# Kernel tuning notes

Hardware: AMD Instinct MI355X
Metric: run time of the kernel (lower is better)

The kernel has to match this reference:

```python
import jax, jax.numpy as jnp
import numpy as np

N = 50000
E = 1600000
IN_C = 165
HID = 256
HEADS = 8
OUT_C = 2
NEG_SLOPE = 0.2


def setup_inputs() -> dict:
    key = jax.random.key(0)
    ks = jax.random.split(key, 10)
    x = jax.random.normal(ks[0], (N, IN_C), dtype=jnp.float32)
    edge_index = jax.random.randint(ks[1], (2, E), 0, N, dtype=jnp.int64)
    c1 = HID // HEADS  # 32 per-head channels in layer 1
    W1 = jax.random.normal(ks[2], (IN_C, HEADS * c1), dtype=jnp.float32) * (1.0 / np.sqrt(IN_C))
    att_src1 = jax.random.normal(ks[3], (HEADS, c1), dtype=jnp.float32) * 0.1
    att_dst1 = jax.random.normal(ks[4], (HEADS, c1), dtype=jnp.float32) * 0.1
    b1 = jnp.zeros((HEADS * c1,), dtype=jnp.float32)
    W2 = jax.random.normal(ks[5], (HID, 1 * OUT_C), dtype=jnp.float32) * (1.0 / np.sqrt(HID))
    att_src2 = jax.random.normal(ks[6], (1, OUT_C), dtype=jnp.float32) * 0.1
    att_dst2 = jax.random.normal(ks[7], (1, OUT_C), dtype=jnp.float32) * 0.1
    b2 = jnp.zeros((OUT_C,), dtype=jnp.float32)
    return {"x": x, "edge_index": edge_index, "W1": W1, "att_src1": att_src1,
            "att_dst1": att_dst1, "b1": b1, "W2": W2, "att_src2": att_src2,
            "att_dst2": att_dst2, "b2": b2}


def _gat_conv(x, src, dst, W, att_src, att_dst, bias, heads, concat):
    """PyG GATConv (eval mode, self-loops already appended to src/dst)."""
    n = x.shape[0]
    c = att_src.shape[1]
    h = (x @ W).reshape(n, heads, c)                      # [N, H, C]
    a_src = jnp.einsum('nhc,hc->nh', h, att_src)          # [N, H]
    a_dst = jnp.einsum('nhc,hc->nh', h, att_dst)
    e = a_src[src] + a_dst[dst]                           # [Et, H]
    e = jax.nn.leaky_relu(e, NEG_SLOPE)
    # segment softmax over incoming edges of each dst node
    e_max = jax.ops.segment_max(e, dst, num_segments=n)   # [N, H]
    e_exp = jnp.exp(e - e_max[dst])
    denom = jax.ops.segment_sum(e_exp, dst, num_segments=n)
    alpha = e_exp / denom[dst]                            # [Et, H]
    msg = alpha[:, :, None] * h[src]                      # [Et, H, C]
    out = jax.ops.segment_sum(msg, dst, num_segments=n)   # [N, H, C]
    if concat:
        out = out.reshape(n, heads * c)
    else:
        out = out.mean(axis=1)
    return out + bias


def reference(x, edge_index, W1, att_src1, att_dst1, b1, W2, att_src2, att_dst2, b2):
    n = x.shape[0]
    loops = jnp.arange(n, dtype=edge_index.dtype)
    src = jnp.concatenate([edge_index[0], loops])  # add_self_loops=True (PyG default)
    dst = jnp.concatenate([edge_index[1], loops])
    h = _gat_conv(x, src, dst, W1, att_src1, att_dst1, b1, HEADS, True)
    h = jax.nn.elu(h)
    out = _gat_conv(h, src, dst, W2, att_src2, att_dst2, b2, 1, False)
    return out
```

## Files before the change

### kernel.cpp

```cpp
#include <hip/hip_runtime.h>
#include <hip/hip_bf16.h>
#include <math.h>

#define N_NODES 50000
#define N_EDGES 1600000
#define ET (N_EDGES + N_NODES)
#define IN_C 165
#define HID 256
#define HEADS 8
#define C1 32
#define OUT_C 2
#define NEG_SLOPE 0.2f
#define LOG2E 1.44269504088896f
#define TROWS 32
#define XSTR 36
#define GEMM_BLOCKS ((N_NODES + TROWS - 1) / TROWS)
#define SCB 2048
#define SGRP 256
#define NPP ((N_NODES + 7) / 8)
#define CAPL 96
#define NE4 (N_EDGES / 4)
#define CK 8
#define NCH 21

typedef float f32x2 __attribute__((ext_vector_type(2)));

__device__ inline float lrelu(float v) { return v > 0.f ? v : NEG_SLOPE * v; }
__device__ inline float e2l(float t) { return exp2f(fmaxf(t, NEG_SLOPE * t)); }

__device__ inline unsigned short f32_bf16(float f) {
    unsigned u = __float_as_uint(f);
    return (unsigned short)((u + 0x7FFFu + ((u >> 16) & 1u)) >> 16);
}

__device__ inline float bflo(unsigned u) { return __uint_as_float(u << 16); }
__device__ inline float bfhi(unsigned u) { return __uint_as_float(u & 0xFFFF0000u); }

__device__ __forceinline__ void gemm1_att_block(
        int row0, const float* __restrict__ x, const float* __restrict__ W,
        const float* __restrict__ att_src, const float* __restrict__ att_dst,
        unsigned short* __restrict__ h, float* __restrict__ a_src,
        float* __restrict__ a_dst, float* xs, float* wb) {
    const int tid = threadIdx.x;
    const int nrow = (N_NODES - row0 < TROWS) ? (N_NODES - row0) : TROWS;
    const int lim = nrow * IN_C;
    for (int idx = tid; idx < TROWS * IN_C; idx += 256) {
        int r = idx / IN_C, k = idx - r * IN_C;
        xs[k * XSTR + r] = (idx < lim) ? x[(size_t)row0 * IN_C + idx] : 0.f;
    }
    const int u  = tid & 31;
    const int kr = tid >> 5;
    {
        const float* wsrc = W + (size_t)kr * HID + u * 8;
        float4 pa = *(const float4*)(wsrc);
        float4 pb = *(const float4*)(wsrc + 4);
        *(float4*)(wb + (kr * 64 + u) * 4)      = pa;
        *(float4*)(wb + (kr * 64 + u + 32) * 4) = pb;
    }
    __syncthreads();

    const int tr = tid >> 5;
    const int cq = tid & 31;
    const int c0 = cq * 8;
    float acc[4][8];
    #pragma unroll
    for (int j = 0; j < 4; ++j)
        #pragma unroll
        for (int q = 0; q < 8; ++q) acc[j][q] = 0.f;

    #pragma unroll 2
    for (int c = 0; c < NCH - 1; ++c) {
        int krow = (c + 1) * CK + kr;
        if (krow > IN_C - 1) krow = IN_C - 1;
        const float* wsrc = W + (size_t)krow * HID + u * 8;
        float4 pa = *(const float4*)(wsrc);
        float4 pb = *(const float4*)(wsrc + 4);
        const float* wcur = wb + (c & 1) * (CK * 256);
        const int k0 = c * CK;
        #pragma unroll
        for (int kk = 0; kk < CK; ++kk) {
            float4 xc = *(const float4*)(xs + (k0 + kk) * XSTR + tr * 4);
            float4 a0 = *(const float4*)(wcur + (kk * 64 + cq) * 4);
            float4 a1 = *(const float4*)(wcur + (kk * 64 + cq + 32) * 4);
            #pragma unroll
            for (int j = 0; j < 4; ++j) {
                float xj = (j == 0) ? xc.x : (j == 1) ? xc.y : (j == 2) ? xc.z : xc.w;
                acc[j][0] += xj * a0.x; acc[j][1] += xj * a0.y;
                acc[j][2] += xj * a0.z; acc[j][3] += xj * a0.w;
                acc[j][4] += xj * a1.x; acc[j][5] += xj * a1.y;
                acc[j][6] += xj * a1.z; acc[j][7] += xj * a1.w;
            }
        }
        float* wn = wb + ((c + 1) & 1) * (CK * 256);
        *(float4*)(wn + (kr * 64 + u) * 4)      = pa;
        *(float4*)(wn + (kr * 64 + u + 32) * 4) = pb;
        __syncthreads();
    }
    {
        const float* wcur = wb + ((NCH - 1) & 1) * (CK * 256);
        const int k0 = (NCH - 1) * CK;
        #pragma unroll
        for (int kk = 0; kk < IN_C - (NCH - 1) * CK; ++kk) {
            float4 xc = *(const float4*)(xs + (k0 + kk) * XSTR + tr * 4);
            float4 a0 = *(const float4*)(wcur + (kk * 64 + cq) * 4);
            float4 a1 = *(const float4*)(wcur + (kk * 64 + cq + 32) * 4);
            #pragma unroll
            for (int j = 0; j < 4; ++j) {
                float xj = (j == 0) ? xc.x : (j == 1) ? xc.y : (j == 2) ? xc.z : xc.w;
                acc[j][0] += xj * a0.x; acc[j][1] += xj * a0.y;
                acc[j][2] += xj * a0.z; acc[j][3] += xj * a0.w;
                acc[j][4] += xj * a1.x; acc[j][5] += xj * a1.y;
                acc[j][6] += xj * a1.z; acc[j][7] += xj * a1.w;
            }
        }
    }
    #pragma unroll
    for (int j = 0; j < 4; ++j) {
        int gr = row0 + tr * 4 + j;
        if (gr < N_NODES) {
            unsigned p[4];
            #pragma unroll
            for (int q = 0; q < 4; ++q)
                p[q] = (unsigned)f32_bf16(acc[j][2*q]) |
                       ((unsigned)f32_bf16(acc[j][2*q+1]) << 16);
            *(uint4*)(h + (size_t)gr * HID + c0) = make_uint4(p[0], p[1], p[2], p[3]);
        }
    }
    {
        const int hd = cq >> 2;
        const float* as = att_src + hd * C1 + (cq & 3) * 8;
        const float* ad = att_dst + hd * C1 + (cq & 3) * 8;
        float av[8], dv[8];
        #pragma unroll
        for (int q = 0; q < 2; ++q) {
            float4 a4 = *(const float4*)(as + q * 4);
            float4 d4 = *(const float4*)(ad + q * 4);
            av[q*4+0]=a4.x; av[q*4+1]=a4.y; av[q*4+2]=a4.z; av[q*4+3]=a4.w;
            dv[q*4+0]=d4.x; dv[q*4+1]=d4.y; dv[q*4+2]=d4.z; dv[q*4+3]=d4.w;
        }
        float ps[4], pd[4];
        #pragma unroll
        for (int j = 0; j < 4; ++j) {
            float s = 0.f, d = 0.f;
            #pragma unroll
            for (int q = 0; q < 8; ++q) {
                s += acc[j][q] * av[q];
                d += acc[j][q] * dv[q];
            }
            ps[j] = s; pd[j] = d;
        }
        #pragma unroll
        for (int off = 1; off <= 2; off <<= 1) {
            #pragma unroll
            for (int j = 0; j < 4; ++j) {
                ps[j] += __shfl_xor(ps[j], off);
                pd[j] += __shfl_xor(pd[j], off);
            }
        }
        if ((cq & 3) == 0) {
            #pragma unroll
            for (int j = 0; j < 4; ++j) {
                int gr = row0 + tr * 4 + j;
                if (gr < N_NODES) {
                    a_src[gr * 8 + hd] = ps[j] * LOG2E;
                    a_dst[gr * 8 + hd] = pd[j] * LOG2E;
                }
            }
        }
    }
}

__global__ __launch_bounds__(256) void fusedAB_kernel(
        const float* __restrict__ x, const float* __restrict__ W,
        const float* __restrict__ att_src, const float* __restrict__ att_dst,
        unsigned short* __restrict__ h, float* __restrict__ a_src,
        float* __restrict__ a_dst,
        const int* __restrict__ src, const int* __restrict__ dst,
        int* __restrict__ deg, unsigned short* __restrict__ csr) {
    __shared__ float xs[IN_C * XSTR];
    __shared__ float wlds[2 * CK * 256];
    if (blockIdx.x < GEMM_BLOCKS) {
        gemm1_att_block(blockIdx.x * TROWS, x, W, att_src, att_dst,
                        h, a_src, a_dst, xs, wlds);
    } else {
        const int sb  = blockIdx.x - GEMM_BLOCKS;
        const int cls = sb & 7;
        const int blk = sb >> 3;
        const int lo = cls * NPP;
        const int hi = (lo + NPP < N_NODES) ? lo + NPP : N_NODES;
        const int t = blk * 256 + threadIdx.x;
        if (t < hi - lo) {
            int d = lo + t;
            int slot = atomicAdd(&deg[d], 1);
            csr[(size_t)d * CAPL + slot] = (unsigned short)d;
        }
        const int4* dst4 = (const int4*)dst;
        for (int uu = t; uu < NE4; uu += SGRP * 256) {
            int4 dv = dst4[uu];
            #pragma unroll
            for (int j = 0; j < 4; ++j) {
                int d = (j == 0) ? dv.x : (j == 1) ? dv.y : (j == 2) ? dv.z : dv.w;
                if (d >= lo && d < hi) {
                    int slot = atomicAdd(&deg[d], 1);
                    csr[(size_t)d * CAPL + slot] = (unsigned short)src[4 * uu + j];
                }
            }
        }
    }
}

__global__ __launch_bounds__(256) void agg1_fused_kernel(
        const int* __restrict__ deg, const unsigned short* __restrict__ csr,
        const float* __restrict__ a_src, const float* __restrict__ a_dst,
        const unsigned short* __restrict__ h1, const float* __restrict__ bias1,
        const float* __restrict__ W2,
        const float* __restrict__ as2, const float* __restrict__ ad2,
        float4* __restrict__ pk, float* __restrict__ a2d) {
    int wid = (blockIdx.x * 256 + threadIdx.x) >> 6;
    int l = threadIdx.x & 63;
    if (wid >= N_NODES) return;
    const int el = l >> 5;
    const int q  = l & 31;
    const int hd = q >> 2;
    const int ch = q * 8;
    const unsigned short* lst = csr + (size_t)wid * CAPL;
    const int n = deg[wid];
    const float ad_p = a_dst[wid * 8 + hd];
    float den = 0.f;
    f32x2 ac0 = {0.f, 0.f}, ac1 = {0.f, 0.f}, ac2 = {0.f, 0.f}, ac3 = {0.f, 0.f};
    int i = 0;
    for (; i + 16 <= n; i += 16) {
        int s[8];
        #pragma unroll
        for (int j = 0; j < 8; ++j) s[j] = lst[i + 2 * j + el];
        uint4 v[8];
        #pragma unroll
        for (int j = 0; j < 8; ++j)
            v[j] = *(const uint4*)(h1 + (size_t)s[j] * HID + ch);
        float w[8];
        #pragma unroll
        for (int j = 0; j < 8; ++j)
            w[j] = e2l(a_src[s[j] * 8 + hd] + ad_p);
        #pragma unroll
        for (int j = 0; j < 8; ++j) {
            den += w[j];
            f32x2 w2 = {w[j], w[j]};
            ac0 += w2 * (f32x2){bflo(v[j].x), bfhi(v[j].x)};
            ac1 += w2 * (f32x2){bflo(v[j].y), bfhi(v[j].y)};
            ac2 += w2 * (f32x2){bflo(v[j].z), bfhi(v[j].z)};
            ac3 += w2 * (f32x2){bflo(v[j].w), bfhi(v[j].w)};
        }
    }
    for (; i < n; i += 8) {
        int s[4]; float mk[4];
        #pragma unroll
        for (int j = 0; j < 4; ++j) {
            int e = i + 2 * j + el;
            mk[j] = (e < n) ? 1.f : 0.f;
            s[j] = lst[(e < n) ? e : (n - 1)];
        }
        uint4 v[4];
        #pragma unroll
        for (int j = 0; j < 4; ++j)
            v[j] = *(const uint4*)(h1 + (size_t)s[j] * HID + ch);
        float w[4];
        #pragma unroll
        for (int j = 0; j < 4; ++j)
            w[j] = mk[j] * e2l(a_src[s[j] * 8 + hd] + ad_p);
        #pragma unroll
        for (int j = 0; j < 4; ++j) {
            den += w[j];
            f32x2 w2 = {w[j], w[j]};
            ac0 += w2 * (f32x2){bflo(v[j].x), bfhi(v[j].x)};
            ac1 += w2 * (f32x2){bflo(v[j].y), bfhi(v[j].y)};
            ac2 += w2 * (f32x2){bflo(v[j].z), bfhi(v[j].z)};
            ac3 += w2 * (f32x2){bflo(v[j].w), bfhi(v[j].w)};
        }
    }
    float accs[8] = {ac0.x, ac0.y, ac1.x, ac1.y, ac2.x, ac2.y, ac3.x, ac3.y};
    den += __shfl_xor(den, 32);
    #pragma unroll
    for (int k = 0; k < 8; ++k) accs[k] += __shfl_xor(accs[k], 32);

    const float inv = 1.f / den;
    float4 bva = *(const float4*)(bias1 + ch);
    float4 bvb = *(const float4*)(bias1 + ch + 4);
    float o[8];
    o[0] = accs[0] * inv + bva.x; o[1] = accs[1] * inv + bva.y;
    o[2] = accs[2] * inv + bva.z; o[3] = accs[3] * inv + bva.w;
    o[4] = accs[4] * inv + bvb.x; o[5] = accs[5] * inv + bvb.y;
    o[6] = accs[6] * inv + bvb.z; o[7] = accs[7] * inv + bvb.w;
    #pragma unroll
    for (int k = 0; k < 8; ++k) o[k] = o[k] > 0.f ? o[k] : expm1f(o[k]);
    const float* wv = W2 + q * 16;
    float4 w0 = *(const float4*)(wv);
    float4 w1 = *(const float4*)(wv + 4);
    float4 w2 = *(const float4*)(wv + 8);
    float4 w3 = *(const float4*)(wv + 12);
    float p0 = o[0]*w0.x + o[1]*w0.z + o[2]*w1.x + o[3]*w1.z
             + o[4]*w2.x + o[5]*w2.z + o[6]*w3.x + o[7]*w3.z;
    float p1 = o[0]*w0.y + o[1]*w0.w + o[2]*w1.y + o[3]*w1.w
             + o[4]*w2.y + o[5]*w2.w + o[6]*w3.y + o[7]*w3.w;
    #pragma unroll
    for (int off = 16; off; off >>= 1) {
        p0 += __shfl_xor(p0, off);
        p1 += __shfl_xor(p1, off);
    }
    if (l == 0) {
        pk[wid] = make_float4(p0, p1, (p0 * as2[0] + p1 * as2[1]) * LOG2E, 0.f);
        a2d[wid] = (p0 * ad2[0] + p1 * ad2[1]) * LOG2E;
    }
}

__global__ __launch_bounds__(256) void agg2_fused_kernel(
        const int* __restrict__ deg, const unsigned short* __restrict__ csr,
        const float4* __restrict__ pk, const float* __restrict__ a2d,
        const float* __restrict__ b2, float* __restrict__ out) {
    int t = blockIdx.x * 256 + threadIdx.x;
    int node = t >> 4;
    int l = t & 15;
    if (node >= N_NODES) return;
    const unsigned short* lst = csr + (size_t)node * CAPL;
    const int n = deg[node];
    const float adv = a2d[node];
    float sm = 0.f, acc0 = 0.f, acc1 = 0.f;
    for (int i = l; i < n; i += 64) {
        int s[4]; float mk[4];
        #pragma unroll
        for (int j = 0; j < 4; ++j) {
            int e = i + 16 * j;
            mk[j] = (e < n) ? 1.f : 0.f;
            s[j] = lst[(e < n) ? e : (n - 1)];
        }
        float4 pv[4];
        #pragma unroll
        for (int j = 0; j < 4; ++j) pv[j] = pk[s[j]];
        #pragma unroll
        for (int j = 0; j < 4; ++j) {
            float w = mk[j] * e2l(pv[j].z + adv);
            sm += w;
            acc0 += w * pv[j].x;
            acc1 += w * pv[j].y;
        }
    }
    #pragma unroll
    for (int off = 8; off; off >>= 1) {
        sm   += __shfl_xor(sm, off);
        acc0 += __shfl_xor(acc0, off);
        acc1 += __shfl_xor(acc1, off);
    }
    if (l == 0) {
        *(float2*)(out + node * 2) =
            make_float2(acc0 / sm + b2[0], acc1 / sm + b2[1]);
    }
}

extern "C" void kernel_launch(void* const* d_in, const int* in_sizes, int n_in,
                              void* d_out, int out_size, void* d_ws, size_t ws_size,
                              hipStream_t stream) {
    (void)in_sizes; (void)n_in; (void)out_size; (void)ws_size;
    const float* x        = (const float*)d_in[0];
    const int*   ei       = (const int*)d_in[1];
    const float* W1       = (const float*)d_in[2];
    const float* att_src1 = (const float*)d_in[3];
    const float* att_dst1 = (const float*)d_in[4];
    const float* b1       = (const float*)d_in[5];
    const float* W2       = (const float*)d_in[6];
    const float* att_src2 = (const float*)d_in[7];
    const float* att_dst2 = (const float*)d_in[8];
    const float* b2       = (const float*)d_in[9];
    float* out = (float*)d_out;

    const int* src = ei;
    const int* dst = ei + N_EDGES;

    char* ws = (char*)d_ws;
    size_t off = 0;
    unsigned short* h1 = (unsigned short*)(ws + off);
    off += (size_t)N_NODES * HID * 2;
    float* a_src1 = (float*)(ws + off); off += (size_t)N_NODES * HEADS * 4;
    float* a_dst1 = (float*)(ws + off); off += (size_t)N_NODES * HEADS * 4;
    float4* pk = (float4*)(ws + off); off += (size_t)N_NODES * 16;
    float* a2d = (float*)(ws + off); off += (size_t)N_NODES * 4;
    int* deg    = (int*)(ws + off); off += (size_t)N_NODES * 4;
    unsigned short* csr = (unsigned short*)(ws + off);
    off += (size_t)N_NODES * CAPL * 2;

    hipMemsetAsync(deg, 0, (size_t)N_NODES * 4, stream);

    const int NW = (N_NODES * 64 + 255) / 256;

    fusedAB_kernel<<<GEMM_BLOCKS + SCB, 256, 0, stream>>>(
        x, W1, att_src1, att_dst1, h1, a_src1, a_dst1, src, dst, deg, csr);

    agg1_fused_kernel<<<NW, 256, 0, stream>>>(
        deg, csr, a_src1, a_dst1, h1, b1, W2, att_src2, att_dst2, pk, a2d);

    agg2_fused_kernel<<<(N_NODES * 16 + 255) / 256, 256, 0, stream>>>(
        deg, csr, pk, a2d, b2, out);
}
```

Before: 338.9 us.

## Replace FP32 scalar layer-1 GEMM with split-bf16 MFMA and folded attention projections

Moves the x@W1 GEMM from FP32 FMA loops to 32x32x16 bf16 MFMA instructions. Both operands are split into hi and lo bf16 parts and three products are summed to stay close to FP32 accuracy. A new prep kernel packs W1 into an MFMA fragment layout. It also precomputes W1·att_src and W1·att_dst so the attention logits come from an extra MFMA on one wave, not from a reduction over the output. This costs an extra kernel launch, a per-block x split in LDS, and uncoalesced scalar bf16 stores of h.

```diff
diff --git a/kernel.cpp b/kernel.cpp
--- a/kernel.cpp
+++ b/kernel.cpp
@@ -13,17 +13,24 @@
 #define NEG_SLOPE 0.2f
 #define LOG2E 1.44269504088896f
 #define TROWS 32
-#define XSTR 36
 #define GEMM_BLOCKS ((N_NODES + TROWS - 1) / TROWS)
 #define SCB 2048
 #define SGRP 256
 #define NPP ((N_NODES + 7) / 8)
 #define CAPL 96
 #define NE4 (N_EDGES / 4)
-#define CK 8
-#define NCH 21
+
+#define NSTEP 11
+#define BIMG_BYTES ((size_t)NSTEP * 16384)
+#define WAIMG_BYTES ((size_t)NSTEP * 2048)
+#define WT (NSTEP * 512)
+#define WPB ((WT + 255) / 256)
+#define WAT (176 * 16)
+#define WAB ((WAT + 255) / 256)
 
 typedef float f32x2 __attribute__((ext_vector_type(2)));
+typedef short s16x8 __attribute__((ext_vector_type(8)));
+typedef float f32x16 __attribute__((ext_vector_type(16)));
 
 __device__ inline float lrelu(float v) { return v > 0.f ? v : NEG_SLOPE * v; }
 __device__ inline float e2l(float t) { return exp2f(fmaxf(t, NEG_SLOPE * t)); }
@@ -35,153 +42,165 @@
 
 __device__ inline float bflo(unsigned u) { return __uint_as_float(u << 16); }
 __device__ inline float bfhi(unsigned u) { return __uint_as_float(u & 0xFFFF0000u); }
-
-__device__ __forceinline__ void gemm1_att_block(
-        int row0, const float* __restrict__ x, const float* __restrict__ W,
+__device__ inline float bf2f(unsigned short b) { return __uint_as_float(((unsigned)b) << 16); }
+
+__global__ __launch_bounds__(256) void prep_kernel(
+        const float* __restrict__ W,
         const float* __restrict__ att_src, const float* __restrict__ att_dst,
+        unsigned short* __restrict__ bImg, unsigned short* __restrict__ waImg) {
+    if (blockIdx.x < WPB) {
+        int g2 = blockIdx.x * 256 + threadIdx.x;
+        if (g2 >= WT) return;
+        int s = g2 >> 9;
+        int r9 = g2 & 511;
+        int kg = r9 >> 8, nsub = (r9 >> 5) & 7, c32 = r9 & 31;
+        int col = nsub * 32 + c32;
+        int k0 = s * 16 + kg * 8;
+        unsigned short hb[8], lb[8];
+        #pragma unroll
+        for (int i = 0; i < 8; ++i) {
+            int k = k0 + i;
+            float v = (k < IN_C) ? W[(size_t)k * HID + col] : 0.f;
+            hb[i] = f32_bf16(v);
+            lb[i] = f32_bf16(v - bf2f(hb[i]));
+        }
+        unsigned ph[4], pl[4];
+        #pragma unroll
+        for (int q = 0; q < 4; ++q) {
+            ph[q] = (unsigned)hb[2*q] | ((unsigned)hb[2*q+1] << 16);
+            pl[q] = (unsigned)lb[2*q] | ((unsigned)lb[2*q+1] << 16);
+        }
+        unsigned short* base = bImg + (size_t)s * 8192
+                             + ((nsub * 2 + kg) * 32 + c32) * 8;
+        *(uint4*)(base)        = make_uint4(ph[0], ph[1], ph[2], ph[3]);
+        *(uint4*)(base + 4096) = make_uint4(pl[0], pl[1], pl[2], pl[3]);
+    } else {
+        int g2 = (blockIdx.x - WPB) * 256 + threadIdx.x;
+        if (g2 >= WAT) return;
+        int k = g2 >> 4, j = g2 & 15;
+        int head = j >> 1;
+        float dotv = 0.f;
+        if (k < IN_C) {
+            const float* wr = W + (size_t)k * HID + head * 32;
+            const float* at = ((j & 1) ? att_dst : att_src) + head * 32;
+            #pragma unroll
+            for (int c = 0; c < 32; c += 4) {
+                float4 wv = *(const float4*)(wr + c);
+                float4 av = *(const float4*)(at + c);
+                dotv += wv.x*av.x + wv.y*av.y + wv.z*av.z + wv.w*av.w;
+            }
+        }
+        unsigned short dh = f32_bf16(dotv);
+        unsigned short dl = f32_bf16(dotv - bf2f(dh));
+        int s = k >> 4, kk = k & 15, kg = kk >> 3, i = kk & 7;
+        unsigned short* base = waImg + (size_t)s * 1024 + (kg * 32 + j) * 8 + i;
+        base[0]   = dh;
+        base[512] = dl;
+    }
+}
+
+__device__ __forceinline__ void gemm_mfma_block(
+        int b, const float* __restrict__ x,
+        const unsigned short* __restrict__ bImg,
+        const unsigned short* __restrict__ waImg,
         unsigned short* __restrict__ h, float* __restrict__ a_src,
-        float* __restrict__ a_dst, float* xs, float* wb) {
+        float* __restrict__ a_dst, unsigned short* asr) {
     const int tid = threadIdx.x;
-    const int nrow = (N_NODES - row0 < TROWS) ? (N_NODES - row0) : TROWS;
-    const int lim = nrow * IN_C;
-    for (int idx = tid; idx < TROWS * IN_C; idx += 256) {
-        int r = idx / IN_C, k = idx - r * IN_C;
-        xs[k * XSTR + r] = (idx < lim) ? x[(size_t)row0 * IN_C + idx] : 0.f;
-    }
-    const int u  = tid & 31;
-    const int kr = tid >> 5;
-    {
-        const float* wsrc = W + (size_t)kr * HID + u * 8;
-        float4 pa = *(const float4*)(wsrc);
-        float4 pb = *(const float4*)(wsrc + 4);
-        *(float4*)(wb + (kr * 64 + u) * 4)      = pa;
-        *(float4*)(wb + (kr * 64 + u + 32) * 4) = pb;
+    const int w = tid >> 6, l = tid & 63;
+    const int half = l >> 5, ln = l & 31;
+    const int row0 = b * TROWS;
+    for (int g = tid; g < 704; g += 256) {
+        int o = g >> 5, row = g & 31;
+        int s = o >> 1, kg = o & 1;
+        int node = row0 + row;
+        int k0 = o * 8;
+        unsigned short hb[8], lb[8];
+        #pragma unroll
+        for (int i = 0; i < 8; ++i) {
+            int k = k0 + i;
+            float v = (node < N_NODES && k < IN_C) ? x[(size_t)node * IN_C + k] : 0.f;
+            hb[i] = f32_bf16(v);
+            lb[i] = f32_bf16(v - bf2f(hb[i]));
+        }
+        unsigned ph[4], pl[4];
+        #pragma unroll
+        for (int q = 0; q < 4; ++q) {
+            ph[q] = (unsigned)hb[2*q] | ((unsigned)hb[2*q+1] << 16);
+            pl[q] = (unsigned)lb[2*q] | ((unsigned)lb[2*q+1] << 16);
+        }
+        unsigned short* base = asr + s * 1024 + (kg * 32 + row) * 8;
+        *(uint4*)(base)       = make_uint4(ph[0], ph[1], ph[2], ph[3]);
+        *(uint4*)(base + 512) = make_uint4(pl[0], pl[1], pl[2], pl[3]);
     }
     __syncthreads();
 
-    const int tr = tid >> 5;
-    const int cq = tid & 31;
-    const int c0 = cq * 8;
-    float acc[4][8];
-    #pragma unroll
-    for (int j = 0; j < 4; ++j)
-        #pragma unroll
-        for (int q = 0; q < 8; ++q) acc[j][q] = 0.f;
-
-    #pragma unroll 2
-    for (int c = 0; c < NCH - 1; ++c) {
-        int krow = (c + 1) * CK + kr;
-        if (krow > IN_C - 1) krow = IN_C - 1;
-        const float* wsrc = W + (size_t)krow * HID + u * 8;
-        float4 pa = *(const float4*)(wsrc);
-        float4 pb = *(const float4*)(wsrc + 4);
-        const float* wcur = wb + (c & 1) * (CK * 256);
-        const int k0 = c * CK;
-        #pragma unroll
-        for (int kk = 0; kk < CK; ++kk) {
-            float4 xc = *(const float4*)(xs + (k0 + kk) * XSTR + tr * 4);
-            float4 a0 = *(const float4*)(wcur + (kk * 64 + cq) * 4);
-            float4 a1 = *(const float4*)(wcur + (kk * 64 + cq + 32) * 4);
-            #pragma unroll
-            for (int j = 0; j < 4; ++j) {
-                float xj = (j == 0) ? xc.x : (j == 1) ? xc.y : (j == 2) ? xc.z : xc.w;
-                acc[j][0] += xj * a0.x; acc[j][1] += xj * a0.y;
-                acc[j][2] += xj * a0.z; acc[j][3] += xj * a0.w;
-                acc[j][4] += xj * a1.x; acc[j][5] += xj * a1.y;
-                acc[j][6] += xj * a1.z; acc[j][7] += xj * a1.w;
+    f32x16 acc0, acc1, accA;
+    #pragma unroll
+    for (int r = 0; r < 16; ++r) { acc0[r] = 0.f; acc1[r] = 0.f; accA[r] = 0.f; }
+    const int ns0 = 2 * w, ns1 = 2 * w + 1;
+    const int afo = (half * 32 + ln) * 8;
+    const int fo0 = ((ns0 * 2 + half) * 32 + ln) * 8;
+    const int fo1 = ((ns1 * 2 + half) * 32 + ln) * 8;
+    for (int s = 0; s < NSTEP; ++s) {
+        const unsigned short* ab = asr + s * 1024;
+        s16x8 a_h = *(const s16x8*)(ab + afo);
+        s16x8 a_l = *(const s16x8*)(ab + 512 + afo);
+        const unsigned short* bb = bImg + (size_t)s * 8192;
+        s16x8 bh0 = *(const s16x8*)(bb + fo0);
+        s16x8 bh1 = *(const s16x8*)(bb + fo1);
+        s16x8 bl0 = *(const s16x8*)(bb + 4096 + fo0);
+        s16x8 bl1 = *(const s16x8*)(bb + 4096 + fo1);
+        acc0 = __builtin_amdgcn_mfma_f32_32x32x16_bf16(a_h, bh0, acc0, 0, 0, 0);
+        acc1 = __builtin_amdgcn_mfma_f32_32x32x16_bf16(a_h, bh1, acc1, 0, 0, 0);
+        acc0 = __builtin_amdgcn_mfma_f32_32x32x16_bf16(a_h, bl0, acc0, 0, 0, 0);
+        acc1 = __builtin_amdgcn_mfma_f32_32x32x16_bf16(a_h, bl1, acc1, 0, 0, 0);
+        acc0 = __builtin_amdgcn_mfma_f32_32x32x16_bf16(a_l, bh0, acc0, 0, 0, 0);
+        acc1 = __builtin_amdgcn_mfma_f32_32x32x16_bf16(a_l, bh1, acc1, 0, 0, 0);
+        if (w == 0) {
+            const unsigned short* wb = waImg + (size_t)s * 1024;
+            s16x8 wah = *(const s16x8*)(wb + afo);
+            s16x8 wal = *(const s16x8*)(wb + 512 + afo);
+            accA = __builtin_amdgcn_mfma_f32_32x32x16_bf16(a_h, wah, accA, 0, 0, 0);
+            accA = __builtin_amdgcn_mfma_f32_32x32x16_bf16(a_h, wal, accA, 0, 0, 0);
+            accA = __builtin_amdgcn_mfma_f32_32x32x16_bf16(a_l, wah, accA, 0, 0, 0);
+        }
+    }
+    #pragma unroll
+    for (int t = 0; t < 2; ++t) {
+        const int colg = w * 64 + t * 32 + ln;
+        #pragma unroll
+        for (int r = 0; r < 16; ++r) {
+            int row = (r & 3) + 8 * (r >> 2) + 4 * half;
+            int gr = row0 + row;
+            if (gr < N_NODES) {
+                float a = t ? acc1[r] : acc0[r];
+                h[(size_t)gr * HID + colg] = f32_bf16(a);
             }
         }
-        float* wn = wb + ((c + 1) & 1) * (CK * 256);
-        *(float4*)(wn + (kr * 64 + u) * 4)      = pa;
-        *(float4*)(wn + (kr * 64 + u + 32) * 4) = pb;
-        __syncthreads();
-    }
-    {
-        const float* wcur = wb + ((NCH - 1) & 1) * (CK * 256);
-        const int k0 = (NCH - 1) * CK;
-        #pragma unroll
-        for (int kk = 0; kk < IN_C - (NCH - 1) * CK; ++kk) {
-            float4 xc = *(const float4*)(xs + (k0 + kk) * XSTR + tr * 4);
-            float4 a0 = *(const float4*)(wcur + (kk * 64 + cq) * 4);
-            float4 a1 = *(const float4*)(wcur + (kk * 64 + cq + 32) * 4);
-            #pragma unroll
-            for (int j = 0; j < 4; ++j) {
-                float xj = (j == 0) ? xc.x : (j == 1) ? xc.y : (j == 2) ? xc.z : xc.w;
-                acc[j][0] += xj * a0.x; acc[j][1] += xj * a0.y;
-                acc[j][2] += xj * a0.z; acc[j][3] += xj * a0.w;
-                acc[j][4] += xj * a1.x; acc[j][5] += xj * a1.y;
-                acc[j][6] += xj * a1.z; acc[j][7] += xj * a1.w;
-            }
-        }
-    }
-    #pragma unroll
-    for (int j = 0; j < 4; ++j) {
-        int gr = row0 + tr * 4 + j;
-        if (gr < N_NODES) {
-            unsigned p[4];
-            #pragma unroll
-            for (int q = 0; q < 4; ++q)
-                p[q] = (unsigned)f32_bf16(acc[j][2*q]) |
-                       ((unsigned)f32_bf16(acc[j][2*q+1]) << 16);
-            *(uint4*)(h + (size_t)gr * HID + c0) = make_uint4(p[0], p[1], p[2], p[3]);
-        }
-    }
-    {
-        const int hd = cq >> 2;
-        const float* as = att_src + hd * C1 + (cq & 3) * 8;
-        const float* ad = att_dst + hd * C1 + (cq & 3) * 8;
-        float av[8], dv[8];
-        #pragma unroll
-        for (int q = 0; q < 2; ++q) {
-            float4 a4 = *(const float4*)(as + q * 4);
-            float4 d4 = *(const float4*)(ad + q * 4);
-            av[q*4+0]=a4.x; av[q*4+1]=a4.y; av[q*4+2]=a4.z; av[q*4+3]=a4.w;
-            dv[q*4+0]=d4.x; dv[q*4+1]=d4.y; dv[q*4+2]=d4.z; dv[q*4+3]=d4.w;
-        }
-        float ps[4], pd[4];
-        #pragma unroll
-        for (int j = 0; j < 4; ++j) {
-            float s = 0.f, d = 0.f;
-            #pragma unroll
-            for (int q = 0; q < 8; ++q) {
-                s += acc[j][q] * av[q];
-                d += acc[j][q] * dv[q];
-            }
-            ps[j] = s; pd[j] = d;
-        }
-        #pragma unroll
-        for (int off = 1; off <= 2; off <<= 1) {
-            #pragma unroll
-            for (int j = 0; j < 4; ++j) {
-                ps[j] += __shfl_xor(ps[j], off);
-                pd[j] += __shfl_xor(pd[j], off);
-            }
-        }
-        if ((cq & 3) == 0) {
-            #pragma unroll
-            for (int j = 0; j < 4; ++j) {
-                int gr = row0 + tr * 4 + j;
-                if (gr < N_NODES) {
-                    a_src[gr * 8 + hd] = ps[j] * LOG2E;
-                    a_dst[gr * 8 + hd] = pd[j] * LOG2E;
-                }
-            }
+    }
+    if (w == 0 && ln < 16) {
+        int head = ln >> 1;
+        float* ap = (ln & 1) ? a_dst : a_src;
+        #pragma unroll
+        for (int r = 0; r < 16; ++r) {
+            int row = (r & 3) + 8 * (r >> 2) + 4 * half;
+            int gr = row0 + row;
+            if (gr < N_NODES) ap[gr * 8 + head] = accA[r] * LOG2E;
         }
     }
 }
 
 __global__ __launch_bounds__(256) void fusedAB_kernel(
-        const float* __restrict__ x, const float* __restrict__ W,
-        const float* __restrict__ att_src, const float* __restrict__ att_dst,
+        const float* __restrict__ x,
+        const unsigned short* __restrict__ bImg,
+        const unsigned short* __restrict__ waImg,
         unsigned short* __restrict__ h, float* __restrict__ a_src,
         float* __restrict__ a_dst,
         const int* __restrict__ src, const int* __restrict__ dst,
         int* __restrict__ deg, unsigned short* __restrict__ csr) {
-    __shared__ float xs[IN_C * XSTR];
-    __shared__ float wlds[2 * CK * 256];
+    __shared__ unsigned short asr[NSTEP * 1024];
     if (blockIdx.x < GEMM_BLOCKS) {
-        gemm1_att_block(blockIdx.x * TROWS, x, W, att_src, att_dst,
-                        h, a_src, a_dst, xs, wlds);
+        gemm_mfma_block(blockIdx.x, x, bImg, waImg, h, a_src, a_dst, asr);
     } else {
         const int sb  = blockIdx.x - GEMM_BLOCKS;
         const int cls = sb & 7;
@@ -385,13 +404,17 @@
     int* deg    = (int*)(ws + off); off += (size_t)N_NODES * 4;
     unsigned short* csr = (unsigned short*)(ws + off);
     off += (size_t)N_NODES * CAPL * 2;
+    unsigned short* bImg  = (unsigned short*)(ws + off); off += BIMG_BYTES;
+    unsigned short* waImg = (unsigned short*)(ws + off); off += WAIMG_BYTES;
 
     hipMemsetAsync(deg, 0, (size_t)N_NODES * 4, stream);
 
     const int NW = (N_NODES * 64 + 255) / 256;
 
+    prep_kernel<<<WPB + WAB, 256, 0, stream>>>(W1, att_src1, att_dst1, bImg, waImg);
+
     fusedAB_kernel<<<GEMM_BLOCKS + SCB, 256, 0, stream>>>(
-        x, W1, att_src1, att_dst1, h1, a_src1, a_dst1, src, dst, deg, csr);
+        x, bImg, waImg, h1, a_src1, a_dst1, src, dst, deg, csr);
 
     agg1_fused_kernel<<<NW, 256, 0, stream>>>(
         deg, csr, a_src1, a_dst1, h1, b1, W2, att_src2, att_dst2, pk, a2d);
```

After: 322.1 us. 1.05x faster.
